# Kernel optimization log

Measured on AMD Instinct MI355X. Metric: run time of the kernel, lower is better.

Reference implementation:

```python
import jax, jax.numpy as jnp
import numpy as np

NPOINTS = 512
RADIUS = 0.4
NSAMPLE = 64
BN_EPS = 1e-5


def square_distance(src, dst):
    # src [B,S,3], dst [B,N,3] -> [B,S,N]
    d = -2.0 * jnp.einsum('bsc,bnc->bsn', src, dst)
    d = d + jnp.sum(src * src, -1)[:, :, None]
    d = d + jnp.sum(dst * dst, -1)[:, None, :]
    return d


def fps_single(coord, npoints):
    # coord [N,3]; deterministic start at index 0 (original uses randint)
    N = coord.shape[0]
    init = (jnp.full((N,), 1e10, coord.dtype), jnp.array(0, jnp.int32))
    def step(carry, _):
        distance, farthest = carry
        centroid = coord[farthest]                      # [3]
        dist = jnp.sum((coord - centroid) ** 2, -1)      # [N]
        distance = jnp.minimum(distance, dist)
        return (distance, jnp.argmax(distance).astype(jnp.int32)), farthest
    _, idx = jax.lax.scan(step, init, None, length=npoints)
    return idx  # [npoints]


def ball_query(samples, coord, radius, nsample):
    # samples [B,S,3], coord [B,N,3] -> group_idx [B,S,nsample]
    B, N, _ = coord.shape
    sq = square_distance(samples, coord)                 # [B,S,N]
    base = jnp.arange(N, dtype=jnp.int32)[None, None, :]
    idx = jnp.where(sq > radius * radius, N, base)
    idx = jnp.sort(idx, axis=-1)[:, :, :nsample]
    first = idx[:, :, :1]
    return jnp.where(idx == N, first, idx)


def mlp_bn_relu(h, ws, bs, gammas, betas):
    # h [B,Cin,N]; pointwise conv1d(k=1) = channel matmul, BN over (B,N), ReLU
    for W, b, g, be in zip(ws, bs, gammas, betas):
        h = jnp.einsum('oi,bin->bon', W, h) + b[None, :, None]
        mean = jnp.mean(h, axis=(0, 2), keepdims=True)
        var = jnp.var(h, axis=(0, 2), keepdims=True)
        h = (h - mean) * jax.lax.rsqrt(var + BN_EPS)
        h = h * g[None, :, None] + be[None, :, None]
        h = jax.nn.relu(h)
    return h


def setup_inputs() -> dict:
    key = jax.random.key(0)
    ks = jax.random.split(key, 8)
    B, N = 16, 4096
    sizes = [3, 64, 64, 128]
    inp = {'coord': jax.random.normal(ks[0], (B, N, 3), jnp.float32)}
    for i in range(len(sizes) - 1):
        cin, cout = sizes[i], sizes[i + 1]
        k = jax.random.fold_in(ks[1], i)
        inp[f'w{i}'] = jax.random.normal(k, (cout, cin), jnp.float32) * (1.0 / np.sqrt(cin))
        inp[f'b{i}'] = jnp.zeros((cout,), jnp.float32)
        inp[f'g{i}'] = jnp.ones((cout,), jnp.float32)
        inp[f'be{i}'] = jnp.zeros((cout,), jnp.float32)
    return inp


def reference(coord, w0, b0, g0, be0, w1, b1, g1, be1, w2, b2, g2, be2):
    # 1) farthest point sampling -> centroid indices [B, NPOINTS]
    cent_idx = jax.vmap(lambda c: fps_single(c, NPOINTS))(coord)
    samples = jnp.take_along_axis(coord, cent_idx[:, :, None], axis=1)  # [B,S,3]
    # 2) eps-ball grouping indices [B, S, NSAMPLE]
    group_idx = ball_query(samples, coord, RADIUS, NSAMPLE)
    # 3) pointwise MLP over all points: [B,3,N] -> [B,128,N]
    h = jnp.transpose(coord, (0, 2, 1))
    feats = mlp_bn_relu(h, [w0, w1, w2], [b0, b1, b2], [g0, g1, g2], [be0, be1, be2])
    return group_idx, feats
```

## Files before the change

kernel.cpp:

```cpp
#include <hip/hip_runtime.h>
#include <hip/hip_bf16.h>

#define NB 16
#define NN 4096
#define NPTS 512
#define NSAMP 64
#define BN_EPS 1e-5f
#define INV_BN (1.0f / 65536.0f)
#define NFPS 16
#define NWRK 128
#define NBLK (NFPS + NWRK)

#define SMEM_BYTES 83968

__device__ __forceinline__ void gbar(int* arrive, int target) {
    __syncthreads();
    if (threadIdx.x == 0) {
        __threadfence();
        atomicAdd(arrive, 1);
        while (__hip_atomic_load(arrive, __ATOMIC_RELAXED,
                                 __HIP_MEMORY_SCOPE_AGENT) < target)
            __builtin_amdgcn_s_sleep(2);
        __threadfence();
    }
    __syncthreads();
}

__device__ __forceinline__ unsigned wave_max_dpp(unsigned x) {
    unsigned o;
    o = (unsigned)__builtin_amdgcn_mov_dpp((int)x, 0x111, 0xF, 0xF, true); x = o > x ? o : x;
    o = (unsigned)__builtin_amdgcn_mov_dpp((int)x, 0x112, 0xF, 0xF, true); x = o > x ? o : x;
    o = (unsigned)__builtin_amdgcn_mov_dpp((int)x, 0x114, 0xF, 0xF, true); x = o > x ? o : x;
    o = (unsigned)__builtin_amdgcn_mov_dpp((int)x, 0x118, 0xF, 0xF, true); x = o > x ? o : x;
    o = (unsigned)__builtin_amdgcn_mov_dpp((int)x, 0x142, 0xF, 0xF, true); x = o > x ? o : x;
    o = (unsigned)__builtin_amdgcn_mov_dpp((int)x, 0x143, 0xF, 0xF, true); x = o > x ? o : x;
    return x;
}

__device__ void fps_body(const float* __restrict__ coord, int* __restrict__ cent,
                         unsigned char* sm) {
    float4* sc = (float4*)sm;
    unsigned long long* slot = (unsigned long long*)(sm + 65536);
    const int b = blockIdx.x;
    const float* cb = coord + (size_t)b * NN * 3;
    const int t = threadIdx.x;

    for (int i = t; i < NN; i += 512)
        sc[i] = make_float4(cb[3 * i], cb[3 * i + 1], cb[3 * i + 2], 0.0f);

    float x[8], y[8], z[8], dist[8];
    {
        const float4* g = (const float4*)(cb + 24 * t);
        const float4 v0 = g[0], v1 = g[1], v2 = g[2], v3 = g[3], v4 = g[4], v5 = g[5];
        x[0] = v0.x; y[0] = v0.y; z[0] = v0.z;
        x[1] = v0.w; y[1] = v1.x; z[1] = v1.y;
        x[2] = v1.z; y[2] = v1.w; z[2] = v2.x;
        x[3] = v2.y; y[3] = v2.z; z[3] = v2.w;
        x[4] = v3.x; y[4] = v3.y; z[4] = v3.z;
        x[5] = v3.w; y[5] = v4.x; z[5] = v4.y;
        x[6] = v4.z; y[6] = v4.w; z[6] = v5.x;
        x[7] = v5.y; y[7] = v5.z; z[7] = v5.w;
    }
#pragma unroll
    for (int k = 0; k < 8; ++k) dist[k] = 1e10f;
    const int lane = t & 63;
    const int wid  = t >> 6;
    const int base = t * 8;
    int far = 0;
    __syncthreads();

    for (int it = 0; it < NPTS; ++it) {
        if (t == 0)
            __hip_atomic_store(&cent[b * NPTS + it], far + 1,
                               __ATOMIC_RELAXED, __HIP_MEMORY_SCOPE_AGENT);
        const float4 c = sc[far];
        float d[8];
#pragma unroll
        for (int k = 0; k < 8; ++k) {
            const float dx = x[k] - c.x;
            const float dy = y[k] - c.y;
            const float dz = z[k] - c.z;
            const float dd = __fadd_rn(__fadd_rn(__fmul_rn(dx, dx), __fmul_rn(dy, dy)),
                                       __fmul_rn(dz, dz));
            const float nd = fminf(dist[k], dd);
            dist[k] = nd;
            d[k] = nd;
        }
        float v0 = d[0]; int i0 = 0;
        if (d[1] > v0) { v0 = d[1]; i0 = 1; }
        float v1 = d[2]; int i1 = 2;
        if (d[3] > v1) { v1 = d[3]; i1 = 3; }
        float v2 = d[4]; int i2 = 4;
        if (d[5] > v2) { v2 = d[5]; i2 = 5; }
        float v3 = d[6]; int i3 = 6;
        if (d[7] > v3) { v3 = d[7]; i3 = 7; }
        if (v1 > v0) { v0 = v1; i0 = i1; }
        if (v3 > v2) { v2 = v3; i2 = i3; }
        if (v2 > v0) { v0 = v2; i0 = i2; }
        const unsigned ub = __float_as_uint(v0);
        const unsigned wm = (unsigned)__builtin_amdgcn_readlane((int)wave_max_dpp(ub), 63);
        const unsigned long long tied = __ballot(ub == wm);
        const int lolane = (int)__builtin_ctzll(tied);
        const int widx = __builtin_amdgcn_readlane(base + i0, lolane);
        if (lane == 0)
            slot[(it & 1) * 8 + wid] =
                ((unsigned long long)wm << 32) | (unsigned)(NN - 1 - widx);
        __syncthreads();
        const ulonglong2* sp = (const ulonglong2*)(slot + (it & 1) * 8);
        const ulonglong2 p0 = sp[0], p1 = sp[1], p2 = sp[2], p3 = sp[3];
        unsigned long long mk = p0.x;
        mk = p0.y > mk ? p0.y : mk;
        mk = p1.x > mk ? p1.x : mk;
        mk = p1.y > mk ? p1.y : mk;
        mk = p2.x > mk ? p2.x : mk;
        mk = p2.y > mk ? p2.y : mk;
        mk = p3.x > mk ? p3.x : mk;
        mk = p3.y > mk ? p3.y : mk;
        far = NN - 1 - (int)(mk & 0xffffffffull);
    }
}

__device__ void ball_one(const float* __restrict__ coord, int ci,
                         float* __restrict__ gout, int gw, int lane) {
    const int b = gw >> 9;
    const float* cb = coord + (size_t)b * NN * 3;
    const float sxv = cb[ci * 3 + 0], syv = cb[ci * 3 + 1], szv = cb[ci * 3 + 2];
    const float ssum = __fadd_rn(__fadd_rn(__fmul_rn(sxv, sxv), __fmul_rn(syv, syv)),
                                 __fmul_rn(szv, szv));
    float* out = gout + (size_t)gw * NSAMP;
    int total = 0;
    int first = 0;
    for (int c = 0; c < NN / 64; ++c) {
        const int p = c * 64 + lane;
        const float cx = cb[p * 3 + 0], cyv = cb[p * 3 + 1], cz = cb[p * 3 + 2];
        const float csum = __fadd_rn(__fadd_rn(__fmul_rn(cx, cx), __fmul_rn(cyv, cyv)),
                                     __fmul_rn(cz, cz));
        const float dot = __fadd_rn(__fadd_rn(__fmul_rn(sxv, cx), __fmul_rn(syv, cyv)),
                                    __fmul_rn(szv, cz));
        float dq = __fmul_rn(-2.0f, dot);
        dq = __fadd_rn(dq, ssum);
        dq = __fadd_rn(dq, csum);
        const bool keep = !(dq > 0.16f);
        const unsigned long long mask = __ballot(keep);
        if (total == 0 && mask) first = c * 64 + (int)__builtin_ctzll(mask);
        if (keep) {
            const int rank = total + __popcll(mask & ((1ull << lane) - 1ull));
            if (rank < NSAMP) out[rank] = (float)p;
        }
        total += (int)__popcll(mask);
        if (total >= NSAMP) break;
    }
    if (total < NSAMP) {
        for (int pos = total + lane; pos < NSAMP; pos += 64) out[pos] = (float)first;
    }
}

template <int C>
__device__ void stats_rows(const float* __restrict__ Y, float* __restrict__ stats,
                           int wb, float* red) {
    const int t = threadIdx.x;
    const int lane = t & 63, wv = t >> 6;
    for (int rid = wb; rid < NB * C; rid += NWRK) {
        const float4* row = (const float4*)(Y + (size_t)rid * NN);
        const float4 va = row[t], vb = row[t + 512];
        float s  = va.x + va.y + va.z + va.w + vb.x + vb.y + vb.z + vb.w;
        float s2 = va.x * va.x + va.y * va.y + va.z * va.z + va.w * va.w +
                   vb.x * vb.x + vb.y * vb.y + vb.z * vb.z + vb.w * vb.w;
#pragma unroll
        for (int m = 1; m < 64; m <<= 1) { s += __shfl_xor(s, m); s2 += __shfl_xor(s2, m); }
        if (lane == 0) { red[wv] = s; red[8 + wv] = s2; }
        __syncthreads();
        if (t == 0) {
            float S = 0.0f, S2 = 0.0f;
            for (int w = 0; w < 8; ++w) { S += red[w]; S2 += red[8 + w]; }
            atomicAdd(&stats[2 * (rid & (C - 1))], S);
            atomicAdd(&stats[2 * (rid & (C - 1)) + 1], S2);
        }
        __syncthreads();
    }
}

__device__ void worker_body(const float* __restrict__ coord,
                            const float* __restrict__ w0, const float* __restrict__ b0,
                            const float* __restrict__ g0, const float* __restrict__ be0,
                            const float* __restrict__ w1, const float* __restrict__ b1,
                            const float* __restrict__ g1, const float* __restrict__ be1,
                            const float* __restrict__ w2, const float* __restrict__ b2,
                            const float* __restrict__ g2, const float* __restrict__ be2,
                            float* a1, float* a2, float* feats, float* gout,
                            float* stats1, float* stats2, float* stats3,
                            int* arrive, const int* cent, unsigned char* sm) {
    float* sW  = (float*)sm;
    float* sB  = (float*)(sm + 32768);
    float* sAC = (float*)(sm + 33280);
    float* red = (float*)(sm + 34304);
    const int t = threadIdx.x;
    const int wb = blockIdx.x - NFPS;
    const int gtid = wb * 512 + t;
    const int b = gtid >> 12, n = gtid & 4095;
    int phase = 0;

    for (int i = t; i < 64 * 3; i += 512) sW[i] = w0[i];
    if (t < 64) sB[t] = b0[t];
    __syncthreads();
    {
        const float x0 = coord[(size_t)gtid * 3 + 0];
        const float x1 = coord[(size_t)gtid * 3 + 1];
        const float x2 = coord[(size_t)gtid * 3 + 2];
        float* outp = a1 + (size_t)b * 64 * NN + n;
#pragma unroll 4
        for (int co = 0; co < 64; ++co) {
            float acc = sB[co];
            acc = fmaf(x0, sW[co * 3 + 0], acc);
            acc = fmaf(x1, sW[co * 3 + 1], acc);
            acc = fmaf(x2, sW[co * 3 + 2], acc);
            outp[(size_t)co * NN] = acc;
        }
    }
    gbar(arrive, NWRK * ++phase);
    stats_rows<64>(a1, stats1, wb, red);
    gbar(arrive, NWRK * ++phase);

    for (int i = t; i < 64 * 64; i += 512) sW[i] = w1[i];
    if (t < 64) sB[t] = b1[t];
    if (t >= 256 && t < 320) {
        const int c = t - 256;
        const float mean = stats1[2 * c] * INV_BN;
        const float var  = stats1[2 * c + 1] * INV_BN - mean * mean;
        const float A = g0[c] * rsqrtf(var + BN_EPS);
        sAC[2 * c] = A;
        sAC[2 * c + 1] = be0[c] - mean * A;
    }
    __syncthreads();
    {
        float xv[64];
        const float* in0 = a1 + (size_t)b * 64 * NN + n;
#pragma unroll
        for (int ci = 0; ci < 64; ++ci) {
            const float v = in0[(size_t)ci * NN];
            xv[ci] = fmaxf(fmaf(v, sAC[2 * ci], sAC[2 * ci + 1]), 0.0f);
        }
        float* outp = a2 + (size_t)b * 64 * NN + n;
#pragma unroll 2
        for (int co = 0; co < 64; ++co) {
            float acc = sB[co];
#pragma unroll
            for (int ci = 0; ci < 64; ++ci) acc = fmaf(xv[ci], sW[co * 64 + ci], acc);
            outp[(size_t)co * NN] = acc;
        }
    }
    gbar(arrive, NWRK * ++phase);
    stats_rows<64>(a2, stats2, wb, red);
    gbar(arrive, NWRK * ++phase);

    for (int i = t; i < 128 * 64; i += 512) sW[i] = w2[i];
    if (t < 128) sB[t] = b2[t];
    if (t >= 256 && t < 320) {
        const int c = t - 256;
        const float mean = stats2[2 * c] * INV_BN;
        const float var  = stats2[2 * c + 1] * INV_BN - mean * mean;
        const float A = g1[c] * rsqrtf(var + BN_EPS);
        sAC[2 * c] = A;
        sAC[2 * c + 1] = be1[c] - mean * A;
    }
    __syncthreads();
    {
        float xv[64];
        const float* in0 = a2 + (size_t)b * 64 * NN + n;
#pragma unroll
        for (int ci = 0; ci < 64; ++ci) {
            const float v = in0[(size_t)ci * NN];
            xv[ci] = fmaxf(fmaf(v, sAC[2 * ci], sAC[2 * ci + 1]), 0.0f);
        }
        float* outp = feats + (size_t)b * 128 * NN + n;
#pragma unroll 2
        for (int co = 0; co < 128; ++co) {
            float acc = sB[co];
#pragma unroll
            for (int ci = 0; ci < 64; ++ci) acc = fmaf(xv[ci], sW[co * 64 + ci], acc);
            outp[(size_t)co * NN] = acc;
        }
    }
    gbar(arrive, NWRK * ++phase);
    stats_rows<128>(feats, stats3, wb, red);
    gbar(arrive, NWRK * ++phase);

    if (t < 128) {
        const float mean = stats3[2 * t] * INV_BN;
        const float var  = stats3[2 * t + 1] * INV_BN - mean * mean;
        const float A = g2[t] * rsqrtf(var + BN_EPS);
        sAC[2 * t] = A;
        sAC[2 * t + 1] = be2[t] - mean * A;
    }
    __syncthreads();
    {
        float4* F = (float4*)feats;
        for (int i = gtid; i < NB * 128 * (NN / 4); i += NWRK * 512) {
            const int c = (i >> 10) & 127;
            const float A = sAC[2 * c], Bc = sAC[2 * c + 1];
            float4 v = F[i];
            v.x = fmaxf(fmaf(v.x, A, Bc), 0.0f);
            v.y = fmaxf(fmaf(v.y, A, Bc), 0.0f);
            v.z = fmaxf(fmaf(v.z, A, Bc), 0.0f);
            v.w = fmaxf(fmaf(v.w, A, Bc), 0.0f);
            F[i] = v;
        }
    }

    const int wvg = wb * 8 + (t >> 6);
    const int lane = t & 63;
#pragma unroll 1
    for (int j = 0; j < 8; ++j) {
        const int gw = wvg * 8 + j;
        const int bb = gw >> 9, ss = gw & 511;
        int v = 0;
        if (lane == 0) {
            while ((v = __hip_atomic_load(&cent[bb * NPTS + ss], __ATOMIC_RELAXED,
                                          __HIP_MEMORY_SCOPE_AGENT)) == 0)
                __builtin_amdgcn_s_sleep(2);
        }
        v = __shfl(v, 0);
        ball_one(coord, v - 1, gout, gw, lane);
    }
}

__global__ __launch_bounds__(512) void mega_kernel(
        const float* __restrict__ coord,
        const float* __restrict__ w0, const float* __restrict__ b0,
        const float* __restrict__ g0, const float* __restrict__ be0,
        const float* __restrict__ w1, const float* __restrict__ b1,
        const float* __restrict__ g1, const float* __restrict__ be1,
        const float* __restrict__ w2, const float* __restrict__ b2,
        const float* __restrict__ g2, const float* __restrict__ be2,
        float* a1, float* a2, float* feats, float* gout,
        float* stats1, float* stats2, float* stats3,
        int* arrive, int* cent) {
    __shared__ __align__(16) unsigned char smem[SMEM_BYTES];
    if (blockIdx.x < NFPS) {
        fps_body(coord, cent, smem);
    } else {
        worker_body(coord, w0, b0, g0, be0, w1, b1, g1, be1, w2, b2, g2, be2,
                    a1, a2, feats, gout, stats1, stats2, stats3,
                    arrive, cent, smem);
    }
}

extern "C" void kernel_launch(void* const* d_in, const int* in_sizes, int n_in,
                              void* d_out, int out_size, void* d_ws, size_t ws_size,
                              hipStream_t stream) {
    const float* coord = (const float*)d_in[0];
    const float* w0  = (const float*)d_in[1];
    const float* b0  = (const float*)d_in[2];
    const float* g0  = (const float*)d_in[3];
    const float* be0 = (const float*)d_in[4];
    const float* w1  = (const float*)d_in[5];
    const float* b1  = (const float*)d_in[6];
    const float* g1  = (const float*)d_in[7];
    const float* be1 = (const float*)d_in[8];
    const float* w2  = (const float*)d_in[9];
    const float* b2  = (const float*)d_in[10];
    const float* g2  = (const float*)d_in[11];
    const float* be2 = (const float*)d_in[12];

    float* ws = (float*)d_ws;
    float* stats1 = ws;
    float* stats2 = ws + 128;
    float* stats3 = ws + 256;
    int*   arrive = (int*)(ws + 512);
    int*   cent   = (int*)(ws + 1024);
    float* a1 = (float*)((char*)d_ws + 65536);
    float* a2 = a1 + (size_t)NB * 64 * NN;

    float* gout  = (float*)d_out;
    float* feats = (float*)d_out + (size_t)NB * NPTS * NSAMP;

    hipMemsetAsync(d_ws, 0, 40960, stream);

    mega_kernel<<<NBLK, 512, 0, stream>>>(
        coord, w0, b0, g0, be0, w1, b1, g1, be1, w2, b2, g2, be2,
        a1, a2, feats, gout, stats1, stats2, stats3, arrive, cent);
}
```

Before: 493.8 us.

## Shrink FPS to four waves and publish centroids in batches via progress counter

The FPS block now runs its serial argmax loop on 256 threads with 16 points each instead of 512 threads with 8, which halves the cross-wave reduction and the number of waves joining each barrier. Centroid indices are staged in LDS and flushed to global memory in groups of 16, followed by a release store to a per-batch progress counter. Worker waves poll that counter with acquire semantics instead of spinning on each centroid slot. The aim is to cut per-iteration sync and global-store cost on the critical FPS path, at the price of more serial work per thread and coarser-grained handoff to the ball-query consumers.

```diff
diff --git a/kernel.cpp b/kernel.cpp
--- a/kernel.cpp
+++ b/kernel.cpp
@@ -38,85 +38,92 @@
 }
 
 __device__ void fps_body(const float* __restrict__ coord, int* __restrict__ cent,
-                         unsigned char* sm) {
+                         int* __restrict__ prog, unsigned char* sm) {
     float4* sc = (float4*)sm;
     unsigned long long* slot = (unsigned long long*)(sm + 65536);
+    int* lds_cent = (int*)(sm + 65600);
     const int b = blockIdx.x;
     const float* cb = coord + (size_t)b * NN * 3;
     const int t = threadIdx.x;
 
     for (int i = t; i < NN; i += 512)
         sc[i] = make_float4(cb[3 * i], cb[3 * i + 1], cb[3 * i + 2], 0.0f);
-
-    float x[8], y[8], z[8], dist[8];
-    {
-        const float4* g = (const float4*)(cb + 24 * t);
-        const float4 v0 = g[0], v1 = g[1], v2 = g[2], v3 = g[3], v4 = g[4], v5 = g[5];
-        x[0] = v0.x; y[0] = v0.y; z[0] = v0.z;
-        x[1] = v0.w; y[1] = v1.x; z[1] = v1.y;
-        x[2] = v1.z; y[2] = v1.w; z[2] = v2.x;
-        x[3] = v2.y; y[3] = v2.z; z[3] = v2.w;
-        x[4] = v3.x; y[4] = v3.y; z[4] = v3.z;
-        x[5] = v3.w; y[5] = v4.x; z[5] = v4.y;
-        x[6] = v4.z; y[6] = v4.w; z[6] = v5.x;
-        x[7] = v5.y; y[7] = v5.z; z[7] = v5.w;
-    }
-#pragma unroll
-    for (int k = 0; k < 8; ++k) dist[k] = 1e10f;
-    const int lane = t & 63;
-    const int wid  = t >> 6;
-    const int base = t * 8;
-    int far = 0;
-    __syncthreads();
-
-    for (int it = 0; it < NPTS; ++it) {
-        if (t == 0)
-            __hip_atomic_store(&cent[b * NPTS + it], far + 1,
-                               __ATOMIC_RELAXED, __HIP_MEMORY_SCOPE_AGENT);
-        const float4 c = sc[far];
-        float d[8];
-#pragma unroll
-        for (int k = 0; k < 8; ++k) {
-            const float dx = x[k] - c.x;
-            const float dy = y[k] - c.y;
-            const float dz = z[k] - c.z;
-            const float dd = __fadd_rn(__fadd_rn(__fmul_rn(dx, dx), __fmul_rn(dy, dy)),
-                                       __fmul_rn(dz, dz));
-            const float nd = fminf(dist[k], dd);
-            dist[k] = nd;
-            d[k] = nd;
-        }
-        float v0 = d[0]; int i0 = 0;
-        if (d[1] > v0) { v0 = d[1]; i0 = 1; }
-        float v1 = d[2]; int i1 = 2;
-        if (d[3] > v1) { v1 = d[3]; i1 = 3; }
-        float v2 = d[4]; int i2 = 4;
-        if (d[5] > v2) { v2 = d[5]; i2 = 5; }
-        float v3 = d[6]; int i3 = 6;
-        if (d[7] > v3) { v3 = d[7]; i3 = 7; }
-        if (v1 > v0) { v0 = v1; i0 = i1; }
-        if (v3 > v2) { v2 = v3; i2 = i3; }
-        if (v2 > v0) { v0 = v2; i0 = i2; }
-        const unsigned ub = __float_as_uint(v0);
-        const unsigned wm = (unsigned)__builtin_amdgcn_readlane((int)wave_max_dpp(ub), 63);
-        const unsigned long long tied = __ballot(ub == wm);
-        const int lolane = (int)__builtin_ctzll(tied);
-        const int widx = __builtin_amdgcn_readlane(base + i0, lolane);
-        if (lane == 0)
-            slot[(it & 1) * 8 + wid] =
-                ((unsigned long long)wm << 32) | (unsigned)(NN - 1 - widx);
-        __syncthreads();
-        const ulonglong2* sp = (const ulonglong2*)(slot + (it & 1) * 8);
-        const ulonglong2 p0 = sp[0], p1 = sp[1], p2 = sp[2], p3 = sp[3];
-        unsigned long long mk = p0.x;
-        mk = p0.y > mk ? p0.y : mk;
-        mk = p1.x > mk ? p1.x : mk;
-        mk = p1.y > mk ? p1.y : mk;
-        mk = p2.x > mk ? p2.x : mk;
-        mk = p2.y > mk ? p2.y : mk;
-        mk = p3.x > mk ? p3.x : mk;
-        mk = p3.y > mk ? p3.y : mk;
-        far = NN - 1 - (int)(mk & 0xffffffffull);
+    __syncthreads();
+
+    if (t < 256) {
+        float x[16], y[16], z[16], dist[16];
+#pragma unroll
+        for (int k = 0; k < 16; ++k) {
+            const float4 v = sc[t * 16 + k];
+            x[k] = v.x; y[k] = v.y; z[k] = v.z; dist[k] = 1e10f;
+        }
+        const int lane = t & 63;
+        const int wid  = t >> 6;
+        const int base = t * 16;
+        int far = 0;
+
+        for (int it = 0; it < NPTS; ++it) {
+            if (t == 0) lds_cent[it & 31] = far;
+            if (t == 192 && it && !(it & 15)) {
+                const int bi = it - 16;
+                const int4* lp = (const int4*)(lds_cent + (bi & 31));
+                const int4 a0 = lp[0], a1 = lp[1], a2 = lp[2], a3 = lp[3];
+                int4* gp = (int4*)(cent + b * NPTS + bi);
+                gp[0] = a0; gp[1] = a1; gp[2] = a2; gp[3] = a3;
+                __hip_atomic_store(&prog[b * 16], it, __ATOMIC_RELEASE,
+                                   __HIP_MEMORY_SCOPE_AGENT);
+            }
+            const float4 c = sc[far];
+            float d[16];
+#pragma unroll
+            for (int k = 0; k < 16; ++k) {
+                const float dx = x[k] - c.x;
+                const float dy = y[k] - c.y;
+                const float dz = z[k] - c.z;
+                const float dd = __fadd_rn(__fadd_rn(__fmul_rn(dx, dx), __fmul_rn(dy, dy)),
+                                           __fmul_rn(dz, dz));
+                const float nd = fminf(dist[k], dd);
+                dist[k] = nd;
+                d[k] = nd;
+            }
+            float vv[16]; int ii[16];
+#pragma unroll
+            for (int k = 0; k < 16; ++k) { vv[k] = d[k]; ii[k] = k; }
+#pragma unroll
+            for (int s = 1; s < 16; s <<= 1) {
+#pragma unroll
+                for (int k = 0; k < 16; k += 2 * s) {
+                    if (vv[k + s] > vv[k]) { vv[k] = vv[k + s]; ii[k] = ii[k + s]; }
+                }
+            }
+            const unsigned ub = __float_as_uint(vv[0]);
+            const unsigned wm = (unsigned)__builtin_amdgcn_readlane(
+                (int)wave_max_dpp(ub), 63);
+            const unsigned long long tied = __ballot(ub == wm);
+            const int lolane = (int)__builtin_ctzll(tied);
+            const int widx = __builtin_amdgcn_readlane(base + ii[0], lolane);
+            if (lane == 0)
+                slot[(it & 1) * 4 + wid] =
+                    ((unsigned long long)wm << 32) | (unsigned)(NN - 1 - widx);
+            __syncthreads();
+            const ulonglong2* sp = (const ulonglong2*)(slot + (it & 1) * 4);
+            const ulonglong2 p0 = sp[0], p1 = sp[1];
+            unsigned long long mk = p0.x;
+            mk = p0.y > mk ? p0.y : mk;
+            mk = p1.x > mk ? p1.x : mk;
+            mk = p1.y > mk ? p1.y : mk;
+            far = NN - 1 - (int)(mk & 0xffffffffull);
+        }
+        if (t == 192) {
+            const int4* lp = (const int4*)(lds_cent + (496 & 31));
+            const int4 a0 = lp[0], a1 = lp[1], a2 = lp[2], a3 = lp[3];
+            int4* gp = (int4*)(cent + b * NPTS + 496);
+            gp[0] = a0; gp[1] = a1; gp[2] = a2; gp[3] = a3;
+            __hip_atomic_store(&prog[b * 16], NPTS, __ATOMIC_RELEASE,
+                               __HIP_MEMORY_SCOPE_AGENT);
+        }
+    } else {
+        for (int it = 0; it < NPTS; ++it) __syncthreads();
     }
 }
 
@@ -189,7 +196,8 @@
                             const float* __restrict__ g2, const float* __restrict__ be2,
                             float* a1, float* a2, float* feats, float* gout,
                             float* stats1, float* stats2, float* stats3,
-                            int* arrive, const int* cent, unsigned char* sm) {
+                            int* arrive, const int* cent, const int* prog,
+                            unsigned char* sm) {
     float* sW  = (float*)sm;
     float* sB  = (float*)(sm + 32768);
     float* sAC = (float*)(sm + 33280);
@@ -315,12 +323,14 @@
         const int bb = gw >> 9, ss = gw & 511;
         int v = 0;
         if (lane == 0) {
-            while ((v = __hip_atomic_load(&cent[bb * NPTS + ss], __ATOMIC_RELAXED,
-                                          __HIP_MEMORY_SCOPE_AGENT)) == 0)
-                __builtin_amdgcn_s_sleep(2);
+            while (__hip_atomic_load(&prog[bb * 16], __ATOMIC_ACQUIRE,
+                                     __HIP_MEMORY_SCOPE_AGENT) <= ss)
+                __builtin_amdgcn_s_sleep(16);
+            v = __hip_atomic_load(&cent[bb * NPTS + ss], __ATOMIC_RELAXED,
+                                  __HIP_MEMORY_SCOPE_AGENT);
         }
         v = __shfl(v, 0);
-        ball_one(coord, v - 1, gout, gw, lane);
+        ball_one(coord, v, gout, gw, lane);
     }
 }
 
@@ -334,14 +344,14 @@
         const float* __restrict__ g2, const float* __restrict__ be2,
         float* a1, float* a2, float* feats, float* gout,
         float* stats1, float* stats2, float* stats3,
-        int* arrive, int* cent) {
+        int* arrive, int* cent, int* prog) {
     __shared__ __align__(16) unsigned char smem[SMEM_BYTES];
     if (blockIdx.x < NFPS) {
-        fps_body(coord, cent, smem);
+        fps_body(coord, cent, prog, smem);
     } else {
         worker_body(coord, w0, b0, g0, be0, w1, b1, g1, be1, w2, b2, g2, be2,
                     a1, a2, feats, gout, stats1, stats2, stats3,
-                    arrive, cent, smem);
+                    arrive, cent, prog, smem);
     }
 }
 
@@ -367,6 +377,7 @@
     float* stats2 = ws + 128;
     float* stats3 = ws + 256;
     int*   arrive = (int*)(ws + 512);
+    int*   prog   = (int*)(ws + 768);
     int*   cent   = (int*)(ws + 1024);
     float* a1 = (float*)((char*)d_ws + 65536);
     float* a2 = a1 + (size_t)NB * 64 * NN;
@@ -378,5 +389,5 @@
 
     mega_kernel<<<NBLK, 512, 0, stream>>>(
         coord, w0, b0, g0, be0, w1, b1, g1, be1, w2, b2, g2, be2,
-        a1, a2, feats, gout, stats1, stats2, stats3, arrive, cent);
-}
+        a1, a2, feats, gout, stats1, stats2, stats3, arrive, cent, prog);
+}
```

Measured after the change: 562.2 us. 13.8% more time.
